# Optimization experiments

Measured on AMD Instinct MI355X. Metric: run time of the kernel, lower is better.

Reference implementation:

```python
import jax, jax.numpy as jnp
import numpy as np

B, V, C, H, W, E = 16, 40000, 128, 56, 56, 120000


def setup_inputs() -> dict:
    key = jax.random.key(0)
    ks = jax.random.split(key, 13)
    img_features = jax.random.normal(ks[0], (B, C, H, W), jnp.float32)
    # vert_align expects xy coords in [-1, 1] (grid_sample convention)
    vertex_position = jax.random.uniform(ks[1], (B, V, 3), jnp.float32, -1.0, 1.0)
    vertex_padded = jax.random.normal(ks[2], (B, V, C), jnp.float32) * 0.1
    edges = jax.random.randint(ks[3], (E, 2), 0, V, dtype=jnp.int32)
    s = 1.0 / np.sqrt(C)
    p = {}
    for li in range(1, 4):
        p[f"w0_{li}"] = jax.random.normal(ks[3 + 3 * li - 2], (C, C), jnp.float32) * s
        p[f"b0_{li}"] = jnp.zeros((C,), jnp.float32)
        p[f"w1_{li}"] = jax.random.normal(ks[3 + 3 * li - 1], (C, C), jnp.float32) * s
    return dict(img_features=img_features, vertex_position=vertex_position,
                vertex_padded=vertex_padded, edges=edges, **p)


def vert_align(feats, verts):
    """Bilinear sample feats [B,C,H,W] at verts[..., :2] in [-1,1] (align_corners=True, zero padding)."""
    Bn, Cn, Hn, Wn = feats.shape
    x = (verts[..., 0] + 1.0) * 0.5 * (Wn - 1)  # [B,V]
    y = (verts[..., 1] + 1.0) * 0.5 * (Hn - 1)
    x0 = jnp.floor(x); y0 = jnp.floor(y)
    wx1 = x - x0; wx0 = 1.0 - wx1
    wy1 = y - y0; wy0 = 1.0 - wy1
    f = jnp.transpose(feats, (0, 2, 3, 1))  # [B,H,W,C]
    bidx = jnp.arange(Bn)[:, None]

    def tap(xi, yi, wgt):
        inb = (xi >= 0) & (xi <= Wn - 1) & (yi >= 0) & (yi <= Hn - 1)
        xc = jnp.clip(xi, 0, Wn - 1).astype(jnp.int32)
        yc = jnp.clip(yi, 0, Hn - 1).astype(jnp.int32)
        val = f[bidx, yc, xc]  # [B,V,C] irregular gather
        return val * (wgt * inb)[..., None]

    return (tap(x0, y0, wx0 * wy0) + tap(x0 + 1, y0, wx1 * wy0) +
            tap(x0, y0 + 1, wx0 * wy1) + tap(x0 + 1, y0 + 1, wx1 * wy1))


def graph_conv(x, edges, w0, b0, w1):
    """pytorch3d-style GraphConv: y = x@W0 + b0 + sum_{j in N(i)} x_j @ W1 (undirected edges)."""
    y1 = jnp.einsum('bvc,co->bvo', x, w1)
    i, j = edges[:, 0], edges[:, 1]
    agg = jnp.zeros_like(y1).at[:, i].add(y1[:, j]).at[:, j].add(y1[:, i])
    return jnp.einsum('bvc,co->bvo', x, w0) + b0 + agg


def reference(img_features, vertex_position, vertex_padded, edges,
              w0_1, b0_1, w1_1, w0_2, b0_2, w1_2, w0_3, b0_3, w1_3):
    pix2vert = vert_align(img_features, vertex_position)      # [B,V,C]
    g = pix2vert + vertex_padded
    d = graph_conv(g, edges, w0_1, b0_1, w1_1)
    d1 = graph_conv(d, edges, w0_2, b0_2, w1_2)
    d1 = graph_conv(d1, edges, w0_3, b0_3, w1_3)
    return d + d1
```

## Files before the change

### kernel.cpp

```cpp
#include <hip/hip_runtime.h>
#include <stdint.h>

#define B_ 16
#define V_ 40000
#define C_ 128
#define H_ 56
#define W_ 56
#define E_ 120000
#define M_ (V_*B_)

typedef float f32x4 __attribute__((ext_vector_type(4)));
typedef __bf16 bf16x8 __attribute__((ext_vector_type(8)));

__device__ __align__(16) uint16_t g_bufA[(size_t)M_*C_];
__device__ __align__(16) uint16_t g_bufB[(size_t)M_*C_];
__device__ __align__(16) uint16_t g_bufD[(size_t)M_*C_];
__device__ __align__(16) uint16_t g_bhwc[(size_t)B_*H_*W_*C_];
__device__ __align__(16) uint16_t g_wf[6][C_*C_];
__device__ int g_cnt[V_];
__device__ int g_rowptr[V_+1];
__device__ int g_cursor[V_];
__device__ int g_adj[2*E_];

__device__ inline float bf_lo(uint32_t u){ return __builtin_bit_cast(float, u<<16); }
__device__ inline float bf_hi(uint32_t u){ return __builtin_bit_cast(float, u & 0xffff0000u); }
__device__ inline uint32_t f2bf(float f){ uint32_t u = __builtin_bit_cast(uint32_t,f); return (u + 0x7fffu + ((u>>16)&1u))>>16; }
__device__ inline uint32_t pk2(float lo, float hi){ return f2bf(lo) | (f2bf(hi)<<16); }

__device__ inline uint16_t* big_buf(int s){ return s==0 ? g_bufA : (s==1 ? g_bufB : g_bufD); }

__global__ void k_zero(){
  int i = blockIdx.x*256 + threadIdx.x;
  if (i < V_) g_cnt[i] = 0;
}
__global__ void k_count(const int* __restrict__ ed){
  int e = blockIdx.x*256 + threadIdx.x;
  if (e < E_){
    atomicAdd(&g_cnt[ed[2*e]],1);
    atomicAdd(&g_cnt[ed[2*e+1]],1);
  }
}
__global__ __launch_bounds__(1024) void k_scan(){
  __shared__ int sd[1024];
  __shared__ int s_carry;
  if (threadIdx.x==0) s_carry = 0;
  __syncthreads();
  for (int base=0; base<V_; base+=1024){
    int idx = base + (int)threadIdx.x;
    int vl = (idx<V_)? g_cnt[idx] : 0;
    sd[threadIdx.x] = vl;
    __syncthreads();
    for (int off=1; off<1024; off<<=1){
      int t = 0;
      if ((int)threadIdx.x >= off) t = sd[threadIdx.x-off];
      __syncthreads();
      sd[threadIdx.x] += t;
      __syncthreads();
    }
    int excl = sd[threadIdx.x] - vl + s_carry;
    if (idx<V_){ g_rowptr[idx] = excl; g_cursor[idx] = excl; }
    __syncthreads();
    if (threadIdx.x==0) s_carry += sd[1023];
    __syncthreads();
  }
  if (threadIdx.x==0) g_rowptr[V_] = s_carry;
}
__global__ void k_fill(const int* __restrict__ ed){
  int e = blockIdx.x*256 + threadIdx.x;
  if (e < E_){
    int i = ed[2*e], j = ed[2*e+1];
    int p = atomicAdd(&g_cursor[i],1); g_adj[p] = j;
    int q = atomicAdd(&g_cursor[j],1); g_adj[q] = i;
  }
}

__global__ __launch_bounds__(256) void k_transpose(const float* __restrict__ feat){
  int idx = blockIdx.x*256 + threadIdx.x;
  int c = idx & (C_-1);
  int p = idx >> 7;
  int x = p % W_;
  int q = p / W_;
  int y = q % H_;
  int b = q / H_;
  g_bhwc[idx] = (uint16_t)f2bf(feat[(((size_t)b*C_ + c)*H_ + y)*W_ + x]);
}

__global__ void k_wprep(const float* w0,const float* w1,const float* w2,
                        const float* w3,const float* w4,const float* w5){
  int tid = blockIdx.x*256 + threadIdx.x;
  int lane = tid & 63;
  int ks = (tid>>6)&3;
  int nt = (tid>>8)&7;
  int mat = tid>>11;
  const float* wsrc = w0;
  switch(mat){ case 1: wsrc=w1; break; case 2: wsrc=w2; break;
               case 3: wsrc=w3; break; case 4: wsrc=w4; break;
               case 5: wsrc=w5; break; default: break; }
  int n  = nt*16 + (lane&15);
  int kb = ks*32 + ((lane>>4)&3)*8;
  uint4 o;
  o.x = pk2(wsrc[(kb+0)*C_+n], wsrc[(kb+1)*C_+n]);
  o.y = pk2(wsrc[(kb+2)*C_+n], wsrc[(kb+3)*C_+n]);
  o.z = pk2(wsrc[(kb+4)*C_+n], wsrc[(kb+5)*C_+n]);
  o.w = pk2(wsrc[(kb+6)*C_+n], wsrc[(kb+7)*C_+n]);
  *(uint4*)&g_wf[mat][((nt*4+ks)*64+lane)*8] = o;
}

__global__ __launch_bounds__(256) void k_vertalign(const float* __restrict__ vpos,
                                                   const float* __restrict__ vpad){
  int wid = blockIdx.x*4 + (threadIdx.x>>6);
  int lane = threadIdx.x & 63;
  int v = wid >> 4, b = wid & 15;
  float px = vpos[((size_t)b*V_+v)*3 + 0];
  float py = vpos[((size_t)b*V_+v)*3 + 1];
  float fx = (px+1.f)*0.5f*(float)(W_-1);
  float fy = (py+1.f)*0.5f*(float)(H_-1);
  float x0f = floorf(fx), y0f = floorf(fy);
  float wx1 = fx-x0f, wy1 = fy-y0f;
  float wx0 = 1.f-wx1, wy0 = 1.f-wy1;
  int x0 = (int)x0f, y0 = (int)y0f;
  int c0 = lane*2;
  float a0 = 0.f, a1 = 0.f;
  #pragma unroll
  for (int t=0;t<4;++t){
    int xi = x0 + (t&1), yi = y0 + (t>>1);
    float wt = ((t&1)? wx1 : wx0) * ((t>>1)? wy1 : wy0);
    if (xi<0||xi>=W_||yi<0||yi>=H_) wt = 0.f;
    int xc = min(max(xi,0),W_-1), yc = min(max(yi,0),H_-1);
    uint32_t u = *(const uint32_t*)(g_bhwc + ((size_t)(b*H_+yc)*W_ + xc)*C_ + c0);
    a0 += bf_lo(u)*wt; a1 += bf_hi(u)*wt;
  }
  float2 vp = *(const float2*)(vpad + ((size_t)b*V_+v)*C_ + c0);
  a0 += vp.x;
  a1 += vp.y;
  *(uint32_t*)(g_bufA + ((size_t)v*B_+b)*C_ + c0) = pk2(a0,a1);
}

__global__ __launch_bounds__(256) void k_aggregate(int xsel){
  const uint16_t* __restrict__ x = big_buf(xsel);
  int v = blockIdx.x;
  int t = threadIdx.x;
  int beg = g_rowptr[v], end = g_rowptr[v+1];
  float a0=0,a1=0,a2=0,a3=0,a4=0,a5=0,a6=0,a7=0;
  const size_t off = (size_t)t*8;
  for (int p=beg;p<end;++p){
    int j = g_adj[p];
    uint4 u = *(const uint4*)(x + (size_t)j*(B_*C_) + off);
    a0 += bf_lo(u.x); a1 += bf_hi(u.x);
    a2 += bf_lo(u.y); a3 += bf_hi(u.y);
    a4 += bf_lo(u.z); a5 += bf_hi(u.z);
    a6 += bf_lo(u.w); a7 += bf_hi(u.w);
  }
  uint4 o = { pk2(a0,a1), pk2(a2,a3), pk2(a4,a5), pk2(a6,a7) };
  *(uint4*)(g_bufB + (size_t)v*(B_*C_) + off) = o;
}

union FragCvt { uint4 u; bf16x8 v; };

__global__ __launch_bounds__(256,2) void k_gemm(int conv, int xsel,
                                                const float* __restrict__ bias_f,
                                                int osel, float* __restrict__ outf){
  __shared__ uint16_t lds_w[2*C_*C_];
  const uint16_t* __restrict__ x  = big_buf(xsel);
  const uint16_t* __restrict__ zp = g_bufB;
  {
    const uint4* src = (const uint4*)(&g_wf[2*conv][0]);
    uint4* dst = (uint4*)lds_w;
    #pragma unroll
    for (int i=0;i<16;++i) dst[i*256 + threadIdx.x] = src[i*256 + threadIdx.x];
  }
  __syncthreads();
  const int wv = threadIdx.x>>6, lane = threadIdx.x&63;
  const int quad = lane>>4, l15 = lane&15;
  const int mbase = blockIdx.x*128 + wv*32;

  FragCvt xf[2][4], zf[2][4];
  #pragma unroll
  for (int mt=0;mt<2;++mt)
    #pragma unroll
    for (int ks=0;ks<4;++ks){
      int row = mbase + mt*16 + l15;
      size_t ad = (size_t)row*C_ + ks*32 + quad*8;
      xf[mt][ks].u = *(const uint4*)(x  + ad);
      zf[mt][ks].u = *(const uint4*)(zp + ad);
    }
  f32x4 acc[2][8];
  #pragma unroll
  for (int mt=0;mt<2;++mt)
    #pragma unroll
    for (int nt=0;nt<8;++nt) acc[mt][nt] = (f32x4){0.f,0.f,0.f,0.f};

  const uint16_t* lw0 = lds_w;
  const uint16_t* lw1 = lds_w + C_*C_;
  #pragma unroll
  for (int nt=0;nt<8;++nt){
    #pragma unroll
    for (int ks=0;ks<4;++ks){
      FragCvt w0f, w1f;
      w0f.u = *(const uint4*)&lw0[((nt*4+ks)*64+lane)*8];
      w1f.u = *(const uint4*)&lw1[((nt*4+ks)*64+lane)*8];
      acc[0][nt] = __builtin_amdgcn_mfma_f32_16x16x32_bf16(w0f.v, xf[0][ks].v, acc[0][nt], 0,0,0);
      acc[0][nt] = __builtin_amdgcn_mfma_f32_16x16x32_bf16(w1f.v, zf[0][ks].v, acc[0][nt], 0,0,0);
      acc[1][nt] = __builtin_amdgcn_mfma_f32_16x16x32_bf16(w0f.v, xf[1][ks].v, acc[1][nt], 0,0,0);
      acc[1][nt] = __builtin_amdgcn_mfma_f32_16x16x32_bf16(w1f.v, zf[1][ks].v, acc[1][nt], 0,0,0);
    }
  }
  uint16_t* oint = big_buf(osel==3 ? 0 : osel);
  #pragma unroll
  for (int mt=0;mt<2;++mt){
    int mrow = mbase + mt*16 + l15;
    int vv = (mbase + mt*16) >> 4;
    #pragma unroll
    for (int nt=0;nt<8;++nt){
      int colb = nt*16 + quad*4;
      f32x4 bu = *(const f32x4*)(bias_f + colb);
      float r0 = acc[mt][nt][0] + bu[0];
      float r1 = acc[mt][nt][1] + bu[1];
      float r2 = acc[mt][nt][2] + bu[2];
      float r3 = acc[mt][nt][3] + bu[3];
      if (osel==3){
        uint2 du = *(const uint2*)(g_bufD + (size_t)mrow*C_ + colb);
        r0 += bf_lo(du.x); r1 += bf_hi(du.x); r2 += bf_lo(du.y); r3 += bf_hi(du.y);
        f32x4 o = { r0, r1, r2, r3 };
        *(f32x4*)(outf + ((size_t)l15*V_ + vv)*C_ + colb) = o;
      } else {
        uint2 o = { pk2(r0,r1), pk2(r2,r3) };
        *(uint2*)(oint + (size_t)mrow*C_ + colb) = o;
      }
    }
  }
}

extern "C" void kernel_launch(void* const* d_in, const int* in_sizes, int n_in,
                              void* d_out, int out_size, void* d_ws, size_t ws_size,
                              hipStream_t stream) {
  const float* feat = (const float*)d_in[0];
  const float* vpos = (const float*)d_in[1];
  const float* vpad = (const float*)d_in[2];
  const int*   edges= (const int*)d_in[3];
  const float* w0_1 = (const float*)d_in[4];
  const float* b0_1 = (const float*)d_in[5];
  const float* w1_1 = (const float*)d_in[6];
  const float* w0_2 = (const float*)d_in[7];
  const float* b0_2 = (const float*)d_in[8];
  const float* w1_2 = (const float*)d_in[9];
  const float* w0_3 = (const float*)d_in[10];
  const float* b0_3 = (const float*)d_in[11];
  const float* w1_3 = (const float*)d_in[12];
  float* outp = (float*)d_out;

  hipLaunchKernelGGL(k_zero,      dim3((V_+255)/256), dim3(256), 0, stream);
  hipLaunchKernelGGL(k_count,     dim3((E_+255)/256), dim3(256), 0, stream, edges);
  hipLaunchKernelGGL(k_scan,      dim3(1),            dim3(1024),0, stream);
  hipLaunchKernelGGL(k_fill,      dim3((E_+255)/256), dim3(256), 0, stream, edges);
  hipLaunchKernelGGL(k_transpose, dim3((B_*H_*W_*C_)/256), dim3(256), 0, stream, feat);
  hipLaunchKernelGGL(k_wprep,     dim3(48),           dim3(256), 0, stream,
                     w0_1, w1_1, w0_2, w1_2, w0_3, w1_3);
  hipLaunchKernelGGL(k_vertalign, dim3(M_/4),         dim3(256), 0, stream, vpos, vpad);
  hipLaunchKernelGGL(k_aggregate, dim3(V_),   dim3(256), 0, stream, 0);
  hipLaunchKernelGGL(k_gemm,      dim3(M_/128), dim3(256), 0, stream, 0, 0, b0_1, 2, outp);
  hipLaunchKernelGGL(k_aggregate, dim3(V_),   dim3(256), 0, stream, 2);
  hipLaunchKernelGGL(k_gemm,      dim3(M_/128), dim3(256), 0, stream, 1, 2, b0_2, 0, outp);
  hipLaunchKernelGGL(k_aggregate, dim3(V_),   dim3(256), 0, stream, 0);
  hipLaunchKernelGGL(k_gemm,      dim3(M_/128), dim3(256), 0, stream, 2, 0, b0_3, 3, outp);
}
```

Measured before the change: 1.693 ms.

## Fuse neighbor aggregation into GEMM, parallelize scan, vectorize vert-align

The separate aggregation kernel and its intermediate buffer are removed. Each GEMM block now gathers and sums neighbor rows directly into MFMA operand registers, then runs the W0 and W1 products in two passes that share a halved LDS tile. This cuts the write and re-read of the aggregate buffer and lets occupancy go to 3 blocks per CU. The single-block CSR scan becomes a three-kernel multi-block scan, and vert-align now uses 16-byte loads with one block per vertex. In exchange, the gather latency sits inside the GEMM kernel and there is an extra LDS reload with barriers.

Result: faster. 1.426 ms (-15.8%).

```diff
diff --git a/kernel.cpp b/kernel.cpp
--- a/kernel.cpp
+++ b/kernel.cpp
@@ -13,7 +13,6 @@
 typedef __bf16 bf16x8 __attribute__((ext_vector_type(8)));
 
 __device__ __align__(16) uint16_t g_bufA[(size_t)M_*C_];
-__device__ __align__(16) uint16_t g_bufB[(size_t)M_*C_];
 __device__ __align__(16) uint16_t g_bufD[(size_t)M_*C_];
 __device__ __align__(16) uint16_t g_bhwc[(size_t)B_*H_*W_*C_];
 __device__ __align__(16) uint16_t g_wf[6][C_*C_];
@@ -21,13 +20,14 @@
 __device__ int g_rowptr[V_+1];
 __device__ int g_cursor[V_];
 __device__ int g_adj[2*E_];
+__device__ int g_blksum[64];
 
 __device__ inline float bf_lo(uint32_t u){ return __builtin_bit_cast(float, u<<16); }
 __device__ inline float bf_hi(uint32_t u){ return __builtin_bit_cast(float, u & 0xffff0000u); }
 __device__ inline uint32_t f2bf(float f){ uint32_t u = __builtin_bit_cast(uint32_t,f); return (u + 0x7fffu + ((u>>16)&1u))>>16; }
 __device__ inline uint32_t pk2(float lo, float hi){ return f2bf(lo) | (f2bf(hi)<<16); }
 
-__device__ inline uint16_t* big_buf(int s){ return s==0 ? g_bufA : (s==1 ? g_bufB : g_bufD); }
+__device__ inline uint16_t* big_buf(int s){ return s==0 ? g_bufA : g_bufD; }
 
 __global__ void k_zero(){
   int i = blockIdx.x*256 + threadIdx.x;
@@ -40,30 +40,36 @@
     atomicAdd(&g_cnt[ed[2*e+1]],1);
   }
 }
-__global__ __launch_bounds__(1024) void k_scan(){
+__global__ __launch_bounds__(1024) void k_scan1(){
   __shared__ int sd[1024];
-  __shared__ int s_carry;
-  if (threadIdx.x==0) s_carry = 0;
+  int idx = blockIdx.x*1024 + (int)threadIdx.x;
+  int vl = (idx<V_)? g_cnt[idx] : 0;
+  sd[threadIdx.x] = vl;
   __syncthreads();
-  for (int base=0; base<V_; base+=1024){
-    int idx = base + (int)threadIdx.x;
-    int vl = (idx<V_)? g_cnt[idx] : 0;
-    sd[threadIdx.x] = vl;
+  #pragma unroll
+  for (int off=1; off<1024; off<<=1){
+    int t = ((int)threadIdx.x >= off) ? sd[threadIdx.x-off] : 0;
     __syncthreads();
-    for (int off=1; off<1024; off<<=1){
-      int t = 0;
-      if ((int)threadIdx.x >= off) t = sd[threadIdx.x-off];
-      __syncthreads();
-      sd[threadIdx.x] += t;
-      __syncthreads();
-    }
-    int excl = sd[threadIdx.x] - vl + s_carry;
-    if (idx<V_){ g_rowptr[idx] = excl; g_cursor[idx] = excl; }
+    sd[threadIdx.x] += t;
     __syncthreads();
-    if (threadIdx.x==0) s_carry += sd[1023];
-    __syncthreads();
-  }
-  if (threadIdx.x==0) g_rowptr[V_] = s_carry;
+  }
+  if (idx<V_) g_rowptr[idx] = sd[threadIdx.x] - vl;
+  if (threadIdx.x==1023) g_blksum[blockIdx.x] = sd[1023];
+}
+__global__ void k_scan2(){
+  if (threadIdx.x==0){
+    int s = 0;
+    for (int i=0;i<40;++i){ int t = g_blksum[i]; g_blksum[i] = s; s += t; }
+    g_rowptr[V_] = s;
+  }
+}
+__global__ __launch_bounds__(1024) void k_scan3(){
+  int idx = blockIdx.x*1024 + (int)threadIdx.x;
+  if (idx<V_){
+    int r = g_rowptr[idx] + g_blksum[blockIdx.x];
+    g_rowptr[idx] = r;
+    g_cursor[idx] = r;
+  }
 }
 __global__ void k_fill(const int* __restrict__ ed){
   int e = blockIdx.x*256 + threadIdx.x;
@@ -108,9 +114,10 @@
 
 __global__ __launch_bounds__(256) void k_vertalign(const float* __restrict__ vpos,
                                                    const float* __restrict__ vpad){
-  int wid = blockIdx.x*4 + (threadIdx.x>>6);
-  int lane = threadIdx.x & 63;
-  int v = wid >> 4, b = wid & 15;
+  int v = blockIdx.x;
+  int t = threadIdx.x;
+  int b = t >> 4;
+  int c0 = (t & 15) * 8;
   float px = vpos[((size_t)b*V_+v)*3 + 0];
   float py = vpos[((size_t)b*V_+v)*3 + 1];
   float fx = (px+1.f)*0.5f*(float)(W_-1);
@@ -119,92 +126,145 @@
   float wx1 = fx-x0f, wy1 = fy-y0f;
   float wx0 = 1.f-wx1, wy0 = 1.f-wy1;
   int x0 = (int)x0f, y0 = (int)y0f;
-  int c0 = lane*2;
-  float a0 = 0.f, a1 = 0.f;
-  #pragma unroll
-  for (int t=0;t<4;++t){
-    int xi = x0 + (t&1), yi = y0 + (t>>1);
-    float wt = ((t&1)? wx1 : wx0) * ((t>>1)? wy1 : wy0);
+
+  float4 p0 = *(const float4*)(vpad + ((size_t)b*V_+v)*C_ + c0);
+  float4 p1 = *(const float4*)(vpad + ((size_t)b*V_+v)*C_ + c0 + 4);
+  float a0=p0.x, a1=p0.y, a2=p0.z, a3=p0.w, a4=p1.x, a5=p1.y, a6=p1.z, a7=p1.w;
+  #pragma unroll
+  for (int tap=0;tap<4;++tap){
+    int xi = x0 + (tap&1), yi = y0 + (tap>>1);
+    float wt = ((tap&1)? wx1 : wx0) * ((tap>>1)? wy1 : wy0);
     if (xi<0||xi>=W_||yi<0||yi>=H_) wt = 0.f;
     int xc = min(max(xi,0),W_-1), yc = min(max(yi,0),H_-1);
-    uint32_t u = *(const uint32_t*)(g_bhwc + ((size_t)(b*H_+yc)*W_ + xc)*C_ + c0);
-    a0 += bf_lo(u)*wt; a1 += bf_hi(u)*wt;
-  }
-  float2 vp = *(const float2*)(vpad + ((size_t)b*V_+v)*C_ + c0);
-  a0 += vp.x;
-  a1 += vp.y;
-  *(uint32_t*)(g_bufA + ((size_t)v*B_+b)*C_ + c0) = pk2(a0,a1);
-}
-
-__global__ __launch_bounds__(256) void k_aggregate(int xsel){
-  const uint16_t* __restrict__ x = big_buf(xsel);
-  int v = blockIdx.x;
-  int t = threadIdx.x;
-  int beg = g_rowptr[v], end = g_rowptr[v+1];
-  float a0=0,a1=0,a2=0,a3=0,a4=0,a5=0,a6=0,a7=0;
-  const size_t off = (size_t)t*8;
-  for (int p=beg;p<end;++p){
-    int j = g_adj[p];
-    uint4 u = *(const uint4*)(x + (size_t)j*(B_*C_) + off);
-    a0 += bf_lo(u.x); a1 += bf_hi(u.x);
-    a2 += bf_lo(u.y); a3 += bf_hi(u.y);
-    a4 += bf_lo(u.z); a5 += bf_hi(u.z);
-    a6 += bf_lo(u.w); a7 += bf_hi(u.w);
+    uint4 u = *(const uint4*)(g_bhwc + ((size_t)(b*H_+yc)*W_ + xc)*C_ + c0);
+    a0 += bf_lo(u.x)*wt; a1 += bf_hi(u.x)*wt;
+    a2 += bf_lo(u.y)*wt; a3 += bf_hi(u.y)*wt;
+    a4 += bf_lo(u.z)*wt; a5 += bf_hi(u.z)*wt;
+    a6 += bf_lo(u.w)*wt; a7 += bf_hi(u.w)*wt;
   }
   uint4 o = { pk2(a0,a1), pk2(a2,a3), pk2(a4,a5), pk2(a6,a7) };
-  *(uint4*)(g_bufB + (size_t)v*(B_*C_) + off) = o;
+  *(uint4*)(g_bufA + ((size_t)v*B_+b)*C_ + c0) = o;
 }
 
 union FragCvt { uint4 u; bf16x8 v; };
 
-__global__ __launch_bounds__(256,2) void k_gemm(int conv, int xsel,
+__global__ __launch_bounds__(256,3) void k_conv(int conv, int xsel,
                                                 const float* __restrict__ bias_f,
                                                 int osel, float* __restrict__ outf){
-  __shared__ uint16_t lds_w[2*C_*C_];
-  const uint16_t* __restrict__ x  = big_buf(xsel);
-  const uint16_t* __restrict__ zp = g_bufB;
+  __shared__ uint16_t lds_w[C_*C_];
+  const uint16_t* __restrict__ x = big_buf(xsel);
+
   {
     const uint4* src = (const uint4*)(&g_wf[2*conv][0]);
     uint4* dst = (uint4*)lds_w;
     #pragma unroll
-    for (int i=0;i<16;++i) dst[i*256 + threadIdx.x] = src[i*256 + threadIdx.x];
-  }
-  __syncthreads();
+    for (int i=0;i<8;++i) dst[i*256 + threadIdx.x] = src[i*256 + threadIdx.x];
+  }
+
   const int wv = threadIdx.x>>6, lane = threadIdx.x&63;
   const int quad = lane>>4, l15 = lane&15;
   const int mbase = blockIdx.x*128 + wv*32;
 
-  FragCvt xf[2][4], zf[2][4];
+  FragCvt xf[2][4];
   #pragma unroll
   for (int mt=0;mt<2;++mt)
     #pragma unroll
     for (int ks=0;ks<4;++ks){
-      int row = mbase + mt*16 + l15;
-      size_t ad = (size_t)row*C_ + ks*32 + quad*8;
-      xf[mt][ks].u = *(const uint4*)(x  + ad);
-      zf[mt][ks].u = *(const uint4*)(zp + ad);
-    }
+      size_t ad = (size_t)(mbase + mt*16 + l15)*C_ + ks*32 + quad*8;
+      xf[mt][ks].u = *(const uint4*)(x + ad);
+    }
+
+  uint4 zf[2][4];
+  const uint16_t* xb = x + (size_t)quad*8;
+  #pragma unroll
+  for (int mt=0;mt<2;++mt){
+    int v = (mbase>>4) + mt;
+    int beg = g_rowptr[v], end = g_rowptr[v+1];
+    float a[4][8];
+    #pragma unroll
+    for (int ks=0;ks<4;++ks)
+      #pragma unroll
+      for (int e=0;e<8;++e) a[ks][e] = 0.f;
+    int p = beg;
+    for (; p+1<end; p+=2){
+      int j0 = g_adj[p], j1 = g_adj[p+1];
+      const uint16_t* r0 = xb + ((size_t)j0*B_ + l15)*C_;
+      const uint16_t* r1 = xb + ((size_t)j1*B_ + l15)*C_;
+      uint4 u0[4], u1[4];
+      #pragma unroll
+      for (int ks=0;ks<4;++ks) u0[ks] = *(const uint4*)(r0 + ks*32);
+      #pragma unroll
+      for (int ks=0;ks<4;++ks) u1[ks] = *(const uint4*)(r1 + ks*32);
+      #pragma unroll
+      for (int ks=0;ks<4;++ks){
+        a[ks][0]+=bf_lo(u0[ks].x); a[ks][1]+=bf_hi(u0[ks].x);
+        a[ks][2]+=bf_lo(u0[ks].y); a[ks][3]+=bf_hi(u0[ks].y);
+        a[ks][4]+=bf_lo(u0[ks].z); a[ks][5]+=bf_hi(u0[ks].z);
+        a[ks][6]+=bf_lo(u0[ks].w); a[ks][7]+=bf_hi(u0[ks].w);
+        a[ks][0]+=bf_lo(u1[ks].x); a[ks][1]+=bf_hi(u1[ks].x);
+        a[ks][2]+=bf_lo(u1[ks].y); a[ks][3]+=bf_hi(u1[ks].y);
+        a[ks][4]+=bf_lo(u1[ks].z); a[ks][5]+=bf_hi(u1[ks].z);
+        a[ks][6]+=bf_lo(u1[ks].w); a[ks][7]+=bf_hi(u1[ks].w);
+      }
+    }
+    if (p<end){
+      int j0 = g_adj[p];
+      const uint16_t* r0 = xb + ((size_t)j0*B_ + l15)*C_;
+      #pragma unroll
+      for (int ks=0;ks<4;++ks){
+        uint4 u0 = *(const uint4*)(r0 + ks*32);
+        a[ks][0]+=bf_lo(u0.x); a[ks][1]+=bf_hi(u0.x);
+        a[ks][2]+=bf_lo(u0.y); a[ks][3]+=bf_hi(u0.y);
+        a[ks][4]+=bf_lo(u0.z); a[ks][5]+=bf_hi(u0.z);
+        a[ks][6]+=bf_lo(u0.w); a[ks][7]+=bf_hi(u0.w);
+      }
+    }
+    #pragma unroll
+    for (int ks=0;ks<4;++ks){
+      uint4 z;
+      z.x = pk2(a[ks][0],a[ks][1]);
+      z.y = pk2(a[ks][2],a[ks][3]);
+      z.z = pk2(a[ks][4],a[ks][5]);
+      z.w = pk2(a[ks][6],a[ks][7]);
+      zf[mt][ks] = z;
+    }
+  }
+
   f32x4 acc[2][8];
   #pragma unroll
   for (int mt=0;mt<2;++mt)
     #pragma unroll
     for (int nt=0;nt<8;++nt) acc[mt][nt] = (f32x4){0.f,0.f,0.f,0.f};
 
-  const uint16_t* lw0 = lds_w;
-  const uint16_t* lw1 = lds_w + C_*C_;
+  __syncthreads();
   #pragma unroll
   for (int nt=0;nt<8;++nt){
     #pragma unroll
     for (int ks=0;ks<4;++ks){
-      FragCvt w0f, w1f;
-      w0f.u = *(const uint4*)&lw0[((nt*4+ks)*64+lane)*8];
-      w1f.u = *(const uint4*)&lw1[((nt*4+ks)*64+lane)*8];
-      acc[0][nt] = __builtin_amdgcn_mfma_f32_16x16x32_bf16(w0f.v, xf[0][ks].v, acc[0][nt], 0,0,0);
-      acc[0][nt] = __builtin_amdgcn_mfma_f32_16x16x32_bf16(w1f.v, zf[0][ks].v, acc[0][nt], 0,0,0);
-      acc[1][nt] = __builtin_amdgcn_mfma_f32_16x16x32_bf16(w0f.v, xf[1][ks].v, acc[1][nt], 0,0,0);
-      acc[1][nt] = __builtin_amdgcn_mfma_f32_16x16x32_bf16(w1f.v, zf[1][ks].v, acc[1][nt], 0,0,0);
-    }
-  }
+      FragCvt wf; wf.u = *(const uint4*)&lds_w[((nt*4+ks)*64+lane)*8];
+      acc[0][nt] = __builtin_amdgcn_mfma_f32_16x16x32_bf16(wf.v, xf[0][ks].v, acc[0][nt], 0,0,0);
+      acc[1][nt] = __builtin_amdgcn_mfma_f32_16x16x32_bf16(wf.v, xf[1][ks].v, acc[1][nt], 0,0,0);
+    }
+  }
+  __syncthreads();
+  {
+    const uint4* src = (const uint4*)(&g_wf[2*conv+1][0]);
+    uint4* dst = (uint4*)lds_w;
+    #pragma unroll
+    for (int i=0;i<8;++i) dst[i*256 + threadIdx.x] = src[i*256 + threadIdx.x];
+  }
+  __syncthreads();
+  #pragma unroll
+  for (int nt=0;nt<8;++nt){
+    #pragma unroll
+    for (int ks=0;ks<4;++ks){
+      FragCvt wf; wf.u = *(const uint4*)&lds_w[((nt*4+ks)*64+lane)*8];
+      FragCvt zc0, zc1; zc0.u = zf[0][ks]; zc1.u = zf[1][ks];
+      acc[0][nt] = __builtin_amdgcn_mfma_f32_16x16x32_bf16(wf.v, zc0.v, acc[0][nt], 0,0,0);
+      acc[1][nt] = __builtin_amdgcn_mfma_f32_16x16x32_bf16(wf.v, zc1.v, acc[1][nt], 0,0,0);
+    }
+  }
+
   uint16_t* oint = big_buf(osel==3 ? 0 : osel);
   #pragma unroll
   for (int mt=0;mt<2;++mt){
@@ -251,16 +311,15 @@
 
   hipLaunchKernelGGL(k_zero,      dim3((V_+255)/256), dim3(256), 0, stream);
   hipLaunchKernelGGL(k_count,     dim3((E_+255)/256), dim3(256), 0, stream, edges);
-  hipLaunchKernelGGL(k_scan,      dim3(1),            dim3(1024),0, stream);
+  hipLaunchKernelGGL(k_scan1,     dim3(40),           dim3(1024),0, stream);
+  hipLaunchKernelGGL(k_scan2,     dim3(1),            dim3(64),  0, stream);
+  hipLaunchKernelGGL(k_scan3,     dim3(40),           dim3(1024),0, stream);
   hipLaunchKernelGGL(k_fill,      dim3((E_+255)/256), dim3(256), 0, stream, edges);
   hipLaunchKernelGGL(k_transpose, dim3((B_*H_*W_*C_)/256), dim3(256), 0, stream, feat);
   hipLaunchKernelGGL(k_wprep,     dim3(48),           dim3(256), 0, stream,
                      w0_1, w1_1, w0_2, w1_2, w0_3, w1_3);
-  hipLaunchKernelGGL(k_vertalign, dim3(M_/4),         dim3(256), 0, stream, vpos, vpad);
-  hipLaunchKernelGGL(k_aggregate, dim3(V_),   dim3(256), 0, stream, 0);
-  hipLaunchKernelGGL(k_gemm,      dim3(M_/128), dim3(256), 0, stream, 0, 0, b0_1, 2, outp);
-  hipLaunchKernelGGL(k_aggregate, dim3(V_),   dim3(256), 0, stream, 2);
-  hipLaunchKernelGGL(k_gemm,      dim3(M_/128), dim3(256), 0, stream, 1, 2, b0_2, 0, outp);
-  hipLaunchKernelGGL(k_aggregate, dim3(V_),   dim3(256), 0, stream, 0);
-  hipLaunchKernelGGL(k_gemm,      dim3(M_/128), dim3(256), 0, stream, 2, 0, b0_3, 3, outp);
-}
+  hipLaunchKernelGGL(k_vertalign, dim3(V_),           dim3(256), 0, stream, vpos, vpad);
+  hipLaunchKernelGGL(k_conv,      dim3(M_/128), dim3(256), 0, stream, 0, 0, b0_1, 2, outp);
+  hipLaunchKernelGGL(k_conv,      dim3(M_/128), dim3(256), 0, stream, 1, 2, b0_2, 0, outp);
+  hipLaunchKernelGGL(k_conv,      dim3(M_/128), dim3(256), 0, stream, 2, 0, b0_3, 3, outp);
+}
```
